# Performance work log

Measured on AMD Instinct MI355X. Metric: run time of the kernel, lower is better.

Reference implementation:

```python
import jax, jax.numpy as jnp
import numpy as np

VOL_SHAPE = (160, 192, 160)

def setup_inputs() -> dict:
    key = jax.random.key(0)
    k1, k2 = jax.random.split(key)
    vol = jax.random.normal(k1, (2, *VOL_SHAPE, 1), dtype=jnp.float32)
    trf = jax.random.normal(k2, (2, *VOL_SHAPE, 3), dtype=jnp.float32)
    return {"vol": vol, "trf": trf}

def _warp(vol, trf):
    # vol: [B, X, Y, Z, C]; trf: [B, X, Y, Z, 3] dense displacement field ('ij' indexing)
    B = vol.shape[0]
    shape = vol.shape[1:-1]
    nd = len(shape)
    # sample locations = identity grid + displacement
    grid = jnp.stack(jnp.meshgrid(*[jnp.arange(s, dtype=vol.dtype) for s in shape], indexing='ij'), axis=-1)
    loc = grid[None] + trf  # [B, X, Y, Z, 3]
    max_f = jnp.array([s - 1 for s in shape], dtype=vol.dtype)
    max_i = jnp.array([s - 1 for s in shape], dtype=jnp.int32)
    # fill_value=None -> clamp to volume border (voxelmorph interpn semantics)
    loc = jnp.clip(loc, 0.0, max_f)
    loc0f = jnp.floor(loc)
    loc0 = jnp.clip(loc0f.astype(jnp.int32), 0, max_i)        # lower corner indices
    loc1 = jnp.clip(loc0 + 1, 0, max_i)                       # upper corner indices (clipped)
    d1 = loc1.astype(vol.dtype) - loc                          # weight for lower corner
    d0 = 1.0 - d1                                              # weight for upper corner
    b = jnp.arange(B)[:, None, None, None]
    out = jnp.zeros(vol.shape, dtype=vol.dtype)
    for c in range(2 ** nd):                                   # 8 corners, fixed small loop
        bits = [(c >> d) & 1 for d in range(nd)]
        idx = [loc1[..., d] if bits[d] else loc0[..., d] for d in range(nd)]
        w = jnp.ones(loc.shape[:-1], dtype=vol.dtype)
        for d in range(nd):
            w = w * (d0[..., d] if bits[d] else d1[..., d])
        out = out + w[..., None] * vol[b, idx[0], idx[1], idx[2]]
    return out

def reference(vol, trf):
    return _warp(vol, trf)
```

## Files before the change

### kernel.cpp

```cpp
#include <hip/hip_runtime.h>


#define NXD 160
#define NYD 192
#define NZD 160
#define NVOX (NXD * NYD * NZD)
#define NBATCH 2

#define TXT 8
#define TYT 16
#define TZT 16
#define LXT 16
#define LYT 24
#define LZT 32
#define LDS_N (LXT * LYT * LZT)

#define TILES_X (NXD / TXT)
#define TILES_Y (NYD / TYT)
#define TILES_Z (NZD / TZT)
#define NBLOCKS (NBATCH * TILES_X * TILES_Y * TILES_Z)

typedef float f4 __attribute__((ext_vector_type(4)));

__global__ __launch_bounds__(512)
void warp3d_kernel(const float* __restrict__ vol,
                   const float* __restrict__ trf,
                   float* __restrict__ out) {
    __shared__ float tile[LDS_N];

    int bid = blockIdx.x;
    int tz = bid % TILES_Z;
    int r  = bid / TILES_Z;
    int ty = r % TILES_Y;
    int r2 = r / TILES_Y;
    int tx = r2 % TILES_X;
    int b  = r2 / TILES_X;

    int x0t = tx * TXT, y0t = ty * TYT, z0t = tz * TZT;
    int lox = x0t - 4, loy = y0t - 4, loz = z0t - 8;

    const float* vb = vol + (size_t)b * NVOX;

    int t = threadIdx.x;
    int zq = t & 3;
    int yq = (t >> 2) & 15;
    int xq = t >> 6;
    int x = x0t + xq, y = y0t + yq, zb0 = z0t + zq * 4;
    size_t vox_i = (((size_t)b * NXD + x) * NYD + y) * NZD + zb0;

    const f4* trfv = (const f4*)(trf + vox_i * 3);
    f4 t0 = trfv[0], t1 = trfv[1], t2 = trfv[2];

    bool interior = (lox >= 0) & (lox + LXT <= NXD) &
                    (loy >= 0) & (loy + LYT <= NYD) &
                    (loz >= 0) & (loz + LZT <= NZD);
    if (interior) {
        const float* gbase = vb + ((size_t)(lox * NYD + loy) * NZD + loz);
        int w = t >> 6;
        int l = t & 63;
#pragma unroll
        for (int it = 0; it < 6; ++it) {
            int chunk = it * 8 + w;
            int p = chunk * 256 + l * 4;
            int zi = p & 31;
            int rest = p >> 5;
            int yi = rest % LYT;
            int xi = rest / LYT;
            const float* g = gbase + (size_t)xi * (NYD * NZD) + yi * NZD + zi;
            __builtin_amdgcn_global_load_lds(
                (const __attribute__((address_space(1))) void*)g,
                (__attribute__((address_space(3))) void*)&tile[chunk * 256],
                16, 0, 0);
        }
    } else {
#pragma unroll 4
        for (int it = 0; it < LDS_N / 512; ++it) {
            int e = it * 512 + t;
            int zi = e & 31;
            int rest = e >> 5;
            int yi = rest % LYT;
            int xi = rest / LYT;
            int gx = min(max(lox + xi, 0), NXD - 1);
            int gy = min(max(loy + yi, 0), NYD - 1);
            int gz = min(max(loz + zi, 0), NZD - 1);
            tile[e] = vb[(size_t)(gx * NYD + gy) * NZD + gz];
        }
    }
    __syncthreads();

    float dxa[4] = {t0.x, t0.w, t1.z, t2.y};
    float dya[4] = {t0.y, t1.x, t1.w, t2.z};
    float dza[4] = {t0.z, t1.y, t2.x, t2.w};

    float res[4];
#pragma unroll
    for (int j = 0; j < 4; ++j) {
        float lx = fminf(fmaxf((float)x + dxa[j], 0.0f), (float)(NXD - 1));
        float ly = fminf(fmaxf((float)y + dya[j], 0.0f), (float)(NYD - 1));
        float lz = fminf(fmaxf((float)(zb0 + j) + dza[j], 0.0f), (float)(NZD - 1));
        float fx = floorf(lx), fy = floorf(ly), fz = floorf(lz);
        int x0 = (int)fx, y0 = (int)fy, z0 = (int)fz;
        float wx0 = fminf(fx + 1.0f, (float)(NXD - 1)) - lx;
        float wy0 = fminf(fy + 1.0f, (float)(NYD - 1)) - ly;
        float wz0 = fminf(fz + 1.0f, (float)(NZD - 1)) - lz;

        int ix = x0 - lox, iy = y0 - loy, iz = z0 - loz;
        bool ok = ((unsigned)ix <= LXT - 2) & ((unsigned)iy <= LYT - 2) &
                  ((unsigned)iz <= LZT - 2);
        int a = ok ? ((ix * LYT + iy) * LZT + iz) : 0;

        float v000 = tile[a],                   v001 = tile[a + 1];
        float v010 = tile[a + LZT],             v011 = tile[a + LZT + 1];
        float v100 = tile[a + LYT * LZT],       v101 = tile[a + LYT * LZT + 1];
        float v110 = tile[a + LYT * LZT + LZT], v111 = tile[a + LYT * LZT + LZT + 1];

        if (!ok) {
            int x1 = min(x0 + 1, NXD - 1);
            int y1 = min(y0 + 1, NYD - 1);
            int z1 = min(z0 + 1, NZD - 1);
            size_t o00 = (size_t)(x0 * NYD + y0) * NZD;
            size_t o01 = (size_t)(x0 * NYD + y1) * NZD;
            size_t o10 = (size_t)(x1 * NYD + y0) * NZD;
            size_t o11 = (size_t)(x1 * NYD + y1) * NZD;
            v000 = vb[o00 + z0]; v001 = vb[o00 + z1];
            v010 = vb[o01 + z0]; v011 = vb[o01 + z1];
            v100 = vb[o10 + z0]; v101 = vb[o10 + z1];
            v110 = vb[o11 + z0]; v111 = vb[o11 + z1];
        }

        float wx1 = 1.0f - wx0, wy1 = 1.0f - wy0, wz1 = 1.0f - wz0;
        res[j] = wx0 * (wy0 * (wz0 * v000 + wz1 * v001) +
                        wy1 * (wz0 * v010 + wz1 * v011)) +
                 wx1 * (wy0 * (wz0 * v100 + wz1 * v101) +
                        wy1 * (wz0 * v110 + wz1 * v111));
    }

    f4 o;
    o.x = res[0]; o.y = res[1]; o.z = res[2]; o.w = res[3];
    *(f4*)(out + vox_i) = o;
}

extern "C" void kernel_launch(void* const* d_in, const int* in_sizes, int n_in,
                              void* d_out, int out_size, void* d_ws, size_t ws_size,
                              hipStream_t stream) {
    const float* vol = (const float*)d_in[0];
    const float* trf = (const float*)d_in[1];
    float* out = (float*)d_out;

    warp3d_kernel<<<NBLOCKS, 512, 0, stream>>>(vol, trf, out);
}
```

Measured before the change: 222.6 us.

## Shrink and pad LDS halo tile, batch gathers across voxels, raise occupancy

Shrinks the z halo of the shared-memory tile from 32 to 24, pads rows to 28 floats to spread LDS banks, and replaces the async global-to-LDS loads with plain f4 loads and stores. The per-voxel gather is split into three phases: compute indices, issue all 32 LDS reads, then blend. This lets LDS latency overlap, and launch bounds request 6 waves per SIMD. The smaller tile cuts LDS footprint and halo traffic but sends more displaced samples down the slow global fallback. Dropping the direct-to-LDS path may add register pressure and VGPR traffic.

Result: no change. 223.3 us (+0.3%).

```diff
diff --git a/kernel.cpp b/kernel.cpp
--- a/kernel.cpp
+++ b/kernel.cpp
@@ -10,10 +10,12 @@
 #define TXT 8
 #define TYT 16
 #define TZT 16
-#define LXT 16
-#define LYT 24
-#define LZT 32
-#define LDS_N (LXT * LYT * LZT)
+
+#define LXS 16
+#define LYS 24
+#define LZS 24
+#define LZP 28
+#define LDS_N (LXS * LYS * LZP)
 
 #define TILES_X (NXD / TXT)
 #define TILES_Y (NYD / TYT)
@@ -22,7 +24,7 @@
 
 typedef float f4 __attribute__((ext_vector_type(4)));
 
-__global__ __launch_bounds__(512)
+__global__ __launch_bounds__(512, 6)
 void warp3d_kernel(const float* __restrict__ vol,
                    const float* __restrict__ trf,
                    float* __restrict__ out) {
@@ -37,53 +39,47 @@
     int b  = r2 / TILES_X;
 
     int x0t = tx * TXT, y0t = ty * TYT, z0t = tz * TZT;
-    int lox = x0t - 4, loy = y0t - 4, loz = z0t - 8;
+    int lox = x0t - 4, loy = y0t - 4, loz = z0t - 4;
 
     const float* vb = vol + (size_t)b * NVOX;
+    int t = threadIdx.x;
 
-    int t = threadIdx.x;
-    int zq = t & 3;
-    int yq = (t >> 2) & 15;
-    int xq = t >> 6;
+    int zq = t & 3, yq = (t >> 2) & 15, xq = t >> 6;
     int x = x0t + xq, y = y0t + yq, zb0 = z0t + zq * 4;
     size_t vox_i = (((size_t)b * NXD + x) * NYD + y) * NZD + zb0;
 
     const f4* trfv = (const f4*)(trf + vox_i * 3);
     f4 t0 = trfv[0], t1 = trfv[1], t2 = trfv[2];
 
-    bool interior = (lox >= 0) & (lox + LXT <= NXD) &
-                    (loy >= 0) & (loy + LYT <= NYD) &
-                    (loz >= 0) & (loz + LZT <= NZD);
+    bool interior = (lox >= 0) & (lox + LXS <= NXD) &
+                    (loy >= 0) & (loy + LYS <= NYD) &
+                    (loz >= 0) & (loz + LZS <= NZD);
     if (interior) {
         const float* gbase = vb + ((size_t)(lox * NYD + loy) * NZD + loz);
-        int w = t >> 6;
-        int l = t & 63;
 #pragma unroll
-        for (int it = 0; it < 6; ++it) {
-            int chunk = it * 8 + w;
-            int p = chunk * 256 + l * 4;
-            int zi = p & 31;
-            int rest = p >> 5;
-            int yi = rest % LYT;
-            int xi = rest / LYT;
-            const float* g = gbase + (size_t)xi * (NYD * NZD) + yi * NZD + zi;
-            __builtin_amdgcn_global_load_lds(
-                (const __attribute__((address_space(1))) void*)g,
-                (__attribute__((address_space(3))) void*)&tile[chunk * 256],
-                16, 0, 0);
+        for (int it = 0; it < 5; ++it) {
+            int c = it * 512 + t;
+            if (c < LXS * LYS * (LZS / 4)) {
+                int z4  = (c % 6) * 4;
+                int row = c / 6;
+                int yi  = row % LYS;
+                int xi  = row / LYS;
+                f4 v = *(const f4*)(gbase + (size_t)xi * (NYD * NZD) + yi * NZD + z4);
+                *(f4*)&tile[(xi * LYS + yi) * LZP + z4] = v;
+            }
         }
     } else {
-#pragma unroll 4
-        for (int it = 0; it < LDS_N / 512; ++it) {
+#pragma unroll 3
+        for (int it = 0; it < 18; ++it) {
             int e = it * 512 + t;
-            int zi = e & 31;
-            int rest = e >> 5;
-            int yi = rest % LYT;
-            int xi = rest / LYT;
+            int zi  = e % LZS;
+            int row = e / LZS;
+            int yi  = row % LYS;
+            int xi  = row / LYS;
             int gx = min(max(lox + xi, 0), NXD - 1);
             int gy = min(max(loy + yi, 0), NYD - 1);
             int gz = min(max(loz + zi, 0), NZD - 1);
-            tile[e] = vb[(size_t)(gx * NYD + gy) * NZD + gz];
+            tile[(xi * LYS + yi) * LZP + zi] = vb[(size_t)(gx * NYD + gy) * NZD + gz];
         }
     }
     __syncthreads();
@@ -92,7 +88,8 @@
     float dya[4] = {t0.y, t1.x, t1.w, t2.z};
     float dza[4] = {t0.z, t1.y, t2.x, t2.w};
 
-    float res[4];
+    float wx0a[4], wy0a[4], wz0a[4];
+    int abase[4], pack[4];
 #pragma unroll
     for (int j = 0; j < 4; ++j) {
         float lx = fminf(fmaxf((float)x + dxa[j], 0.0f), (float)(NXD - 1));
@@ -100,21 +97,35 @@
         float lz = fminf(fmaxf((float)(zb0 + j) + dza[j], 0.0f), (float)(NZD - 1));
         float fx = floorf(lx), fy = floorf(ly), fz = floorf(lz);
         int x0 = (int)fx, y0 = (int)fy, z0 = (int)fz;
-        float wx0 = fminf(fx + 1.0f, (float)(NXD - 1)) - lx;
-        float wy0 = fminf(fy + 1.0f, (float)(NYD - 1)) - ly;
-        float wz0 = fminf(fz + 1.0f, (float)(NZD - 1)) - lz;
+        wx0a[j] = fminf(fx + 1.0f, (float)(NXD - 1)) - lx;
+        wy0a[j] = fminf(fy + 1.0f, (float)(NYD - 1)) - ly;
+        wz0a[j] = fminf(fz + 1.0f, (float)(NZD - 1)) - lz;
 
         int ix = x0 - lox, iy = y0 - loy, iz = z0 - loz;
-        bool ok = ((unsigned)ix <= LXT - 2) & ((unsigned)iy <= LYT - 2) &
-                  ((unsigned)iz <= LZT - 2);
-        int a = ok ? ((ix * LYT + iy) * LZT + iz) : 0;
+        bool ok = ((unsigned)ix <= LXS - 2) & ((unsigned)iy <= LYS - 2) &
+                  ((unsigned)iz <= LZS - 2);
+        abase[j] = ok ? ((ix * LYS + iy) * LZP + iz) : 0;
+        pack[j]  = ok ? -1 : (x0 | (y0 << 8) | (z0 << 16));
+    }
 
-        float v000 = tile[a],                   v001 = tile[a + 1];
-        float v010 = tile[a + LZT],             v011 = tile[a + LZT + 1];
-        float v100 = tile[a + LYT * LZT],       v101 = tile[a + LYT * LZT + 1];
-        float v110 = tile[a + LYT * LZT + LZT], v111 = tile[a + LYT * LZT + LZT + 1];
+    float g[4][8];
+#pragma unroll
+    for (int j = 0; j < 4; ++j) {
+        int a = abase[j];
+        g[j][0] = tile[a];                   g[j][1] = tile[a + 1];
+        g[j][2] = tile[a + LZP];             g[j][3] = tile[a + LZP + 1];
+        g[j][4] = tile[a + LYS * LZP];       g[j][5] = tile[a + LYS * LZP + 1];
+        g[j][6] = tile[a + LYS * LZP + LZP]; g[j][7] = tile[a + LYS * LZP + LZP + 1];
+    }
 
-        if (!ok) {
+    float res[4];
+#pragma unroll
+    for (int j = 0; j < 4; ++j) {
+        float v000 = g[j][0], v001 = g[j][1], v010 = g[j][2], v011 = g[j][3];
+        float v100 = g[j][4], v101 = g[j][5], v110 = g[j][6], v111 = g[j][7];
+
+        if (pack[j] != -1) {
+            int x0 = pack[j] & 255, y0 = (pack[j] >> 8) & 255, z0 = (pack[j] >> 16) & 255;
             int x1 = min(x0 + 1, NXD - 1);
             int y1 = min(y0 + 1, NYD - 1);
             int z1 = min(z0 + 1, NZD - 1);
@@ -128,6 +139,7 @@
             v110 = vb[o11 + z0]; v111 = vb[o11 + z1];
         }
 
+        float wx0 = wx0a[j], wy0 = wy0a[j], wz0 = wz0a[j];
         float wx1 = 1.0f - wx0, wy1 = 1.0f - wy0, wz1 = 1.0f - wz0;
         res[j] = wx0 * (wy0 * (wz0 * v000 + wz1 * v001) +
                         wy1 * (wz0 * v010 + wz1 * v011)) +
```
